# Optimization experiments

Measured on AMD Instinct MI355X. Metric: run time of the kernel, lower is better.

The kernel has to match this reference:

```python
import jax, jax.numpy as jnp
import numpy as np

D = 128        # d_model
B = 32         # graphs in batch
NV = 500       # vars per graph -> 2*NV literals per graph
NL = B * 2 * NV            # 32000 literals
NC_G = 2000                # clauses per graph
NC = B * NC_G              # 64000 clauses
K = 3                      # literals per clause
NE = NC * K                # 192000 edges


def setup_inputs() -> dict:
    key = jax.random.key(0)
    ks = jax.random.split(key, 16)
    s = 1.0 / np.sqrt(D)
    inp = {
        'x_unk': jax.random.uniform(ks[0], (NL, D), dtype=jnp.float32),
        'C_w': jax.random.normal(ks[1], (D,), dtype=jnp.float32) * s,
        'C_b': jax.random.normal(ks[2], (D,), dtype=jnp.float32) * s,
        'Wih_lc': jax.random.normal(ks[3], (4 * D, D), dtype=jnp.float32) * s,
        'Whh_lc': jax.random.normal(ks[4], (4 * D, D), dtype=jnp.float32) * s,
        'bih_lc': jax.random.normal(ks[5], (4 * D,), dtype=jnp.float32) * s,
        'bhh_lc': jax.random.normal(ks[6], (4 * D,), dtype=jnp.float32) * s,
        'Wih_cl': jax.random.normal(ks[7], (4 * D, 2 * D), dtype=jnp.float32) * s,
        'Whh_cl': jax.random.normal(ks[8], (4 * D, D), dtype=jnp.float32) * s,
        'bih_cl': jax.random.normal(ks[9], (4 * D,), dtype=jnp.float32) * s,
        'bhh_cl': jax.random.normal(ks[10], (4 * D,), dtype=jnp.float32) * s,
        'out_w': jax.random.normal(ks[11], (D, 1), dtype=jnp.float32) * s,
        'out_b': jax.random.normal(ks[12], (1,), dtype=jnp.float32) * s,
    }
    rng = np.random.default_rng(0)
    # each clause samples K literals within its own graph
    lit_local = rng.integers(0, 2 * NV, size=(B, NC_G, K))
    offs = (np.arange(B) * 2 * NV)[:, None, None]
    inp['lit_idx'] = jnp.asarray((lit_local + offs).reshape(-1), dtype=jnp.int32)
    inp['clause_idx'] = jnp.asarray(np.repeat(np.arange(NC), K), dtype=jnp.int32)
    inp['l_batch'] = jnp.asarray(np.repeat(np.arange(B), 2 * NV), dtype=jnp.int32)
    # literal flip: swap pos/neg halves within each graph
    loc = np.arange(2 * NV)
    flip_local = np.concatenate([loc[NV:], loc[:NV]])
    inp['flip_perm'] = jnp.asarray(((np.arange(B) * 2 * NV)[:, None] + flip_local[None, :]).reshape(-1), dtype=jnp.int32)
    inp['num_iters'] = 4
    return inp


def _lstm_step(x, h, c, Wih, Whh, bih, bhh):
    # PyTorch LSTM cell: gates ordered [i, f, g, o]
    g = x @ Wih.T + h @ Whh.T + (bih + bhh)
    i, f, gg, o = jnp.split(g, 4, axis=-1)
    c2 = jax.nn.sigmoid(f) * c + jax.nn.sigmoid(i) * jnp.tanh(gg)
    h2 = jax.nn.sigmoid(o) * jnp.tanh(c2)
    return h2, c2


def reference(x_unk, C_w, C_b, Wih_lc, Whh_lc, bih_lc, bhh_lc,
              Wih_cl, Whh_cl, bih_cl, bhh_cl, out_w, out_b,
              clause_idx, lit_idx, l_batch, flip_perm, num_iters):
    n_lits = x_unk.shape[0]
    n_clauses = clause_idx.shape[0] // K
    # init embeddings: x_unk ~ U[0,1); x_c = C_init(1) repeated; cell states zero
    h_l, c_l = x_unk, jnp.zeros_like(x_unk)
    h_c = jnp.broadcast_to(C_w + C_b, (n_clauses, D))  # Linear(1,d) on ones(1)
    c_c = jnp.zeros((n_clauses, D), dtype=x_unk.dtype)
    for _ in range(num_iters):
        # lit -> clause: msg = adj_t @ x_l (SpMM via gather+segment_sum)
        msg_c = jax.ops.segment_sum(h_l[lit_idx], clause_idx, num_segments=n_clauses)
        h_c, c_c = _lstm_step(msg_c, h_c, c_c, Wih_lc, Whh_lc, bih_lc, bhh_lc)
        # clause -> lit: msg = adj_t.T @ x_c, concat with flipped literals
        msg_l = jax.ops.segment_sum(h_c[clause_idx], lit_idx, num_segments=n_lits)
        inp = jnp.concatenate([msg_l, h_l[flip_perm]], axis=-1)  # [NL, 2D]
        h_l, c_l = _lstm_step(inp, h_l, c_l, Wih_cl, Whh_cl, bih_cl, bhh_cl)
    votes = h_l @ out_w + out_b  # [NL, 1]
    sums = jax.ops.segment_sum(votes, l_batch, num_segments=B)
    cnts = jax.ops.segment_sum(jnp.ones((n_lits, 1), votes.dtype), l_batch, num_segments=B)
    vote_reduced = sums / cnts  # global_mean_pool
    return vote_reduced, votes, h_l
```

## Files before the change

### kernel.cpp

```cpp
#include <hip/hip_runtime.h>
#include <hip/hip_bf16.h>

#define D     128
#define NLIT  32000
#define NCLA  64000
#define KLIT  3
#define NEDGE 192000
#define BGR   32
#define ITERS 4
#define LITS_PER_GRAPH 1000

typedef _Float16 f16x8 __attribute__((ext_vector_type(8)));
typedef float    f32x4 __attribute__((ext_vector_type(4)));

__device__ __forceinline__ float sigf(float x)  { return 1.f / (1.f + __expf(-x)); }
__device__ __forceinline__ float tanhft(float x){ return 1.f - 2.f / (__expf(2.f * x) + 1.f); }

__device__ __forceinline__ void async_cp16(const void* g, void* l) {
    __builtin_amdgcn_global_load_lds((const __attribute__((address_space(1))) void*)g,
                                     (__attribute__((address_space(3))) void*)l,
                                     16, 0, 0);
}

__global__ void conv_x_kernel(const float* __restrict__ x, _Float16* __restrict__ o) {
    int t = blockIdx.x * blockDim.x + threadIdx.x;
    if (t >= NLIT * 16) return;
    const float* p = x + t * 8;
    f16x8 v;
#pragma unroll
    for (int i = 0; i < 8; ++i) v[i] = (_Float16)p[i];
    *(f16x8*)((_Float16*)o + t * 8) = v;
}

__global__ void conv_wc_kernel(const float* __restrict__ Wih,
                               const float* __restrict__ Whh,
                               _Float16* __restrict__ Wc) {
    int n = blockIdx.x, k = threadIdx.x;
    float v = (k < 128) ? Wih[n * 128 + k] : Whh[n * 128 + k - 128];
    Wc[n * 256 + k] = (_Float16)v;
}

__global__ void conv_wl_kernel(const float* __restrict__ Wih,
                               const float* __restrict__ Whh,
                               _Float16* __restrict__ Wl) {
    int n = blockIdx.x, k = threadIdx.x;
    float v = (k < 256) ? Wih[n * 256 + k] : Whh[n * 128 + k - 256];
    Wl[n * 384 + k] = (_Float16)v;
}

__global__ void conv_bias_kernel(const float* bih_c, const float* bhh_c, float* bc,
                                 const float* bih_l, const float* bhh_l, float* bl,
                                 const float* C_w, const float* C_b,
                                 _Float16* hc0g) {
    int t = threadIdx.x;
    bc[t] = bih_c[t] + bhh_c[t];
    bl[t] = bih_l[t] + bhh_l[t];
    if (t < 128) hc0g[t] = (_Float16)(C_w[t] + C_b[t]);
}

__global__ void count_edges_kernel(const int* __restrict__ lit_idx,
                                   int* __restrict__ counts) {
    int e = blockIdx.x * blockDim.x + threadIdx.x;
    if (e < NEDGE) atomicAdd(&counts[lit_idx[e]], 1);
}

__global__ __launch_bounds__(256)
void block_sum_kernel(const int* __restrict__ counts, int* __restrict__ bsum) {
    int b = blockIdx.x, t = threadIdx.x;
    int v = counts[b * 256 + t];
    int lane = t & 63, w = t >> 6;
#pragma unroll
    for (int off = 32; off > 0; off >>= 1) v += __shfl_down(v, off, 64);
    __shared__ int ws[4];
    if (lane == 0) ws[w] = v;
    __syncthreads();
    if (t == 0) bsum[b] = ws[0] + ws[1] + ws[2] + ws[3];
}

__global__ void scan_bsum_kernel(const int* __restrict__ bsum,
                                 int* __restrict__ ebsum,
                                 int* __restrict__ starts) {
    __shared__ int s[128];
    int t = threadIdx.x;
    int v = (t < 125) ? bsum[t] : 0;
    s[t] = v;
    __syncthreads();
    for (int off = 1; off < 128; off <<= 1) {
        int y = (t >= off) ? s[t - off] : 0;
        __syncthreads();
        s[t] += y;
        __syncthreads();
    }
    if (t < 125) ebsum[t] = s[t] - v;
    if (t == 0) starts[NLIT] = NEDGE;
}

__global__ __launch_bounds__(256)
void scan_write_kernel(const int* __restrict__ counts,
                       const int* __restrict__ ebsum,
                       int* __restrict__ starts,
                       int* __restrict__ cursor) {
    int b = blockIdx.x, t = threadIdx.x;
    int idx = b * 256 + t;
    int v = counts[idx];
    int lane = t & 63, w = t >> 6;
    int x = v;
#pragma unroll
    for (int off = 1; off < 64; off <<= 1) {
        int y = __shfl_up(x, off, 64);
        if (lane >= off) x += y;
    }
    __shared__ int wsum[4];
    if (lane == 63) wsum[w] = x;
    __syncthreads();
    int woff = 0;
#pragma unroll
    for (int i = 0; i < 4; ++i) if (i < w) woff += wsum[i];
    int g = ebsum[b] + woff + x - v;
    starts[idx] = g;
    cursor[idx] = g;
}

__global__ void fill_csr_kernel(const int* __restrict__ lit_idx,
                                const int* __restrict__ clause_idx,
                                int* __restrict__ cursor,
                                int* __restrict__ edge_clause) {
    int e = blockIdx.x * blockDim.x + threadIdx.x;
    if (e < NEDGE) {
        int l = lit_idx[e];
        int pos = atomicAdd(&cursor[l], 1);
        edge_clause[pos] = clause_idx[e];
    }
}

__global__ void gather_msg_kernel(const _Float16* __restrict__ h_c16,
                                  _Float16* __restrict__ msg16,
                                  const int* __restrict__ starts,
                                  const int* __restrict__ edge_clause) {
    int t = blockIdx.x * blockDim.x + threadIdx.x;
    if (t >= NLIT * 16) return;
    int l = t >> 4;
    int off = (t & 15) * 8;
    int s = starts[l], e = starts[l + 1];
    float a[8];
#pragma unroll
    for (int i = 0; i < 8; ++i) a[i] = 0.f;
    for (int j = s; j < e; ++j) {
        f16x8 v = *(const f16x8*)&h_c16[(size_t)edge_clause[j] * D + off];
#pragma unroll
        for (int i = 0; i < 8; ++i) a[i] += (float)v[i];
    }
    f16x8 o;
#pragma unroll
    for (int i = 0; i < 8; ++i) o[i] = (_Float16)a[i];
    *(f16x8*)&msg16[(size_t)l * D + off] = o;
}

__global__ __launch_bounds__(256, 2)
void clause_mfma_kernel(const _Float16* __restrict__ h_l16,
                        const _Float16* __restrict__ h_c_old,
                        _Float16* __restrict__ h_c_new,
                        float* __restrict__ c_c,
                        const _Float16* __restrict__ Wc,
                        const float* __restrict__ bc,
                        const _Float16* __restrict__ hc0g,
                        const int* __restrict__ lit_idx,
                        int first) {
    __shared__ _Float16 Wl[256 * 32];
    __shared__ _Float16 Al[128 * 32];
    __shared__ int      lidx[384];

    const int tid  = threadIdx.x;
    const int w    = tid >> 6;
    const int lane = tid & 63;
    const int qd   = lane >> 4;
    const int ln   = lane & 15;
    const int bx   = blockIdx.x;
    const int c    = bx & 1;
    const int row0 = (bx >> 1) * 128;

    for (int i = tid; i < 384; i += 256) lidx[i] = lit_idx[row0 * 3 + i];

    f32x4 acc[8][4];
#pragma unroll
    for (int R = 0; R < 8; ++R)
#pragma unroll
        for (int g = 0; g < 4; ++g) { acc[R][g][0]=0.f; acc[R][g][1]=0.f; acc[R][g][2]=0.f; acc[R][g][3]=0.f; }

    for (int ch = 0; ch < 8; ++ch) {
        const int k0 = ch * 32;
        __syncthreads();
        {
            const int nbase = w * 128 + c * 64;
#pragma unroll
            for (int j = 0; j < 4; ++j) {
                int r = 16 * j + (lane >> 2);
                async_cp16(Wc + (nbase + r) * 256 + k0 + (lane & 3) * 8,
                           &Wl[(64 * w + 16 * j) * 32]);
            }
        }
        if (ch < 4) {
#pragma unroll
            for (int s2 = 0; s2 < 2; ++s2) {
                int s   = tid + 256 * s2;
                int m   = s >> 2;
                int off = (s & 3) * 8;
                int kk  = k0 + off;
                f16x8 v0 = *(const f16x8*)&h_l16[(size_t)lidx[3 * m + 0] * D + kk];
                f16x8 v1 = *(const f16x8*)&h_l16[(size_t)lidx[3 * m + 1] * D + kk];
                f16x8 v2 = *(const f16x8*)&h_l16[(size_t)lidx[3 * m + 2] * D + kk];
                f16x8 o;
#pragma unroll
                for (int i = 0; i < 8; ++i) o[i] = (_Float16)((float)v0[i] + (float)v1[i] + (float)v2[i]);
                *(f16x8*)&Al[m * 32 + off] = o;
            }
        } else if (first) {
#pragma unroll
            for (int s2 = 0; s2 < 2; ++s2) {
                int s   = tid + 256 * s2;
                int m   = s >> 2;
                int off = (s & 3) * 8;
                f16x8 v = *(const f16x8*)&hc0g[(k0 - 128) + off];
                *(f16x8*)&Al[m * 32 + off] = v;
            }
        } else {
            int m = 32 * w + (lane >> 2);
            async_cp16(h_c_old + (size_t)(row0 + m) * D + (k0 - 128) + (lane & 3) * 8,
                       &Al[(32 * w) * 32]);
            async_cp16(h_c_old + (size_t)(row0 + m + 16) * D + (k0 - 128) + (lane & 3) * 8,
                       &Al[(32 * w + 16) * 32]);
        }
        __syncthreads();
        f16x8 af[8], bf[4];
#pragma unroll
        for (int R = 0; R < 8; ++R)
            af[R] = *(const f16x8*)&Al[(16 * R + ln) * 32 + qd * 8];
#pragma unroll
        for (int g = 0; g < 4; ++g)
            bf[g] = *(const f16x8*)&Wl[(64 * g + 16 * w + ln) * 32 + qd * 8];
#pragma unroll
        for (int R = 0; R < 8; ++R)
#pragma unroll
            for (int g = 0; g < 4; ++g)
                acc[R][g] = __builtin_amdgcn_mfma_f32_16x16x32_f16(af[R], bf[g], acc[R][g], 0, 0, 0);
    }

    const int dcol = c * 64 + 16 * w + ln;
    const float b0 = bc[dcol], b1 = bc[128 + dcol], b2 = bc[256 + dcol], b3 = bc[384 + dcol];
#pragma unroll
    for (int R = 0; R < 8; ++R) {
#pragma unroll
        for (int r = 0; r < 4; ++r) {
            int m = row0 + 16 * R + qd * 4 + r;
            size_t idx = (size_t)m * D + dcol;
            float gi = acc[R][0][r] + b0;
            float gf = acc[R][1][r] + b1;
            float gg = acc[R][2][r] + b2;
            float go = acc[R][3][r] + b3;
            float cn = sigf(gi) * tanhft(gg);
            if (!first) cn += sigf(gf) * c_c[idx];
            float h  = sigf(go) * tanhft(cn);
            c_c[idx]     = cn;
            h_c_new[idx] = (_Float16)h;
        }
    }
}

__global__ __launch_bounds__(256, 2)
void literal_mfma_kernel(const _Float16* __restrict__ h_old16,
                         const _Float16* __restrict__ msg16,
                         _Float16* __restrict__ h_new16,
                         float* __restrict__ h32,
                         float* __restrict__ c_l,
                         const _Float16* __restrict__ Wl384,
                         const float* __restrict__ bl,
                         const int* __restrict__ flip_perm,
                         int first) {
    __shared__ _Float16 Wl[256 * 32];
    __shared__ _Float16 Al[128 * 32];
    __shared__ int      flip_s[128];

    const int tid  = threadIdx.x;
    const int w    = tid >> 6;
    const int lane = tid & 63;
    const int qd   = lane >> 4;
    const int ln   = lane & 15;
    const int bx   = blockIdx.x;
    const int c    = bx & 1;
    const int row0 = (bx >> 1) * 128;

    if (tid < 128) flip_s[tid] = flip_perm[row0 + tid];

    f32x4 acc[8][4];
#pragma unroll
    for (int R = 0; R < 8; ++R)
#pragma unroll
        for (int g = 0; g < 4; ++g) { acc[R][g][0]=0.f; acc[R][g][1]=0.f; acc[R][g][2]=0.f; acc[R][g][3]=0.f; }

    for (int ch = 0; ch < 12; ++ch) {
        const int k0 = ch * 32;
        __syncthreads();
        {
            const int nbase = w * 128 + c * 64;
#pragma unroll
            for (int j = 0; j < 4; ++j) {
                int r = 16 * j + (lane >> 2);
                async_cp16(Wl384 + (nbase + r) * 384 + k0 + (lane & 3) * 8,
                           &Wl[(64 * w + 16 * j) * 32]);
            }
        }
        {
            int m0  = 32 * w + (lane >> 2);
            int sub = (lane & 3) * 8;
            const _Float16 *g0, *g1;
            if (ch < 4) {
                g0 = msg16 + (size_t)(row0 + m0) * D + k0 + sub;
                g1 = msg16 + (size_t)(row0 + m0 + 16) * D + k0 + sub;
            } else if (ch < 8) {
                g0 = h_old16 + (size_t)flip_s[m0] * D + (k0 - 128) + sub;
                g1 = h_old16 + (size_t)flip_s[m0 + 16] * D + (k0 - 128) + sub;
            } else {
                g0 = h_old16 + (size_t)(row0 + m0) * D + (k0 - 256) + sub;
                g1 = h_old16 + (size_t)(row0 + m0 + 16) * D + (k0 - 256) + sub;
            }
            async_cp16(g0, &Al[(32 * w) * 32]);
            async_cp16(g1, &Al[(32 * w + 16) * 32]);
        }
        __syncthreads();
        f16x8 af[8], bf[4];
#pragma unroll
        for (int R = 0; R < 8; ++R)
            af[R] = *(const f16x8*)&Al[(16 * R + ln) * 32 + qd * 8];
#pragma unroll
        for (int g = 0; g < 4; ++g)
            bf[g] = *(const f16x8*)&Wl[(64 * g + 16 * w + ln) * 32 + qd * 8];
#pragma unroll
        for (int R = 0; R < 8; ++R)
#pragma unroll
            for (int g = 0; g < 4; ++g)
                acc[R][g] = __builtin_amdgcn_mfma_f32_16x16x32_f16(af[R], bf[g], acc[R][g], 0, 0, 0);
    }

    const int dcol = c * 64 + 16 * w + ln;
    const float b0 = bl[dcol], b1 = bl[128 + dcol], b2 = bl[256 + dcol], b3 = bl[384 + dcol];
#pragma unroll
    for (int R = 0; R < 8; ++R) {
#pragma unroll
        for (int r = 0; r < 4; ++r) {
            int m = row0 + 16 * R + qd * 4 + r;
            size_t idx = (size_t)m * D + dcol;
            float gi = acc[R][0][r] + b0;
            float gf = acc[R][1][r] + b1;
            float gg = acc[R][2][r] + b2;
            float go = acc[R][3][r] + b3;
            float cn = sigf(gi) * tanhft(gg);
            if (!first) cn += sigf(gf) * c_l[idx];
            float h  = sigf(go) * tanhft(cn);
            c_l[idx]     = cn;
            h_new16[idx] = (_Float16)h;
            if (h32) h32[idx] = h;
        }
    }
}

__global__ __launch_bounds__(256)
void votes_stage1_kernel(const float* __restrict__ h_l,
                         const float* __restrict__ out_w,
                         const float* __restrict__ out_b,
                         float* __restrict__ votes_out) {
    int w    = threadIdx.x >> 6;
    int lane = threadIdx.x & 63;
    int l    = blockIdx.x * 4 + w;
    if (l >= NLIT) return;
    const float2 v = *(const float2*)&h_l[(size_t)l * D + lane * 2];
    const float2 ww = *(const float2*)&out_w[lane * 2];
    float p = v.x * ww.x + v.y * ww.y;
#pragma unroll
    for (int off = 32; off > 0; off >>= 1) p += __shfl_down(p, off, 64);
    if (lane == 0) votes_out[l] = p + out_b[0];
}

__global__ __launch_bounds__(256)
void votes_stage2_kernel(const float* __restrict__ votes,
                         float* __restrict__ out0) {
    int b = blockIdx.x;
    int t = threadIdx.x;
    const float* base = votes + (size_t)b * LITS_PER_GRAPH;
    float s = 0.f;
    for (int i = t; i < LITS_PER_GRAPH; i += 256) s += base[i];
#pragma unroll
    for (int off = 32; off > 0; off >>= 1) s += __shfl_down(s, off, 64);
    __shared__ float ws[4];
    if ((t & 63) == 0) ws[t >> 6] = s;
    __syncthreads();
    if (t == 0) out0[b] = (ws[0] + ws[1] + ws[2] + ws[3]) / (float)LITS_PER_GRAPH;
}

extern "C" void kernel_launch(void* const* d_in, const int* in_sizes, int n_in,
                              void* d_out, int out_size, void* d_ws, size_t ws_size,
                              hipStream_t stream) {
    (void)in_sizes; (void)n_in; (void)out_size; (void)ws_size;

    const float* x_unk  = (const float*)d_in[0];
    const float* C_w    = (const float*)d_in[1];
    const float* C_b    = (const float*)d_in[2];
    const float* Wih_lc = (const float*)d_in[3];
    const float* Whh_lc = (const float*)d_in[4];
    const float* bih_lc = (const float*)d_in[5];
    const float* bhh_lc = (const float*)d_in[6];
    const float* Wih_cl = (const float*)d_in[7];
    const float* Whh_cl = (const float*)d_in[8];
    const float* bih_cl = (const float*)d_in[9];
    const float* bhh_cl = (const float*)d_in[10];
    const float* out_w  = (const float*)d_in[11];
    const float* out_b  = (const float*)d_in[12];
    const int* lit_idx    = (const int*)d_in[13];
    const int* clause_idx = (const int*)d_in[14];
    const int* flip_perm  = (const int*)d_in[16];

    char* W = (char*)d_ws;
    size_t off = 0;
    auto alloc = [&](size_t bytes) { char* p = W + off; off = (off + bytes + 255) & ~(size_t)255; return p; };
    _Float16* h_l16_0 = (_Float16*)alloc((size_t)NLIT * D * 2);
    _Float16* h_l16_1 = (_Float16*)alloc((size_t)NLIT * D * 2);
    _Float16* h_c16_0 = (_Float16*)alloc((size_t)NCLA * D * 2);
    _Float16* h_c16_1 = (_Float16*)alloc((size_t)NCLA * D * 2);
    _Float16* msg16   = (_Float16*)alloc((size_t)NLIT * D * 2);
    float*    c_l     = (float*)  alloc((size_t)NLIT * D * 4);
    float*    c_c     = (float*)  alloc((size_t)NCLA * D * 4);
    _Float16* Wc16    = (_Float16*)alloc(512 * 256 * 2);
    _Float16* Wl16    = (_Float16*)alloc(512 * 384 * 2);
    float*    bc      = (float*)  alloc(512 * 4);
    float*    bl      = (float*)  alloc(512 * 4);
    _Float16* hc0g    = (_Float16*)alloc(128 * 2);
    int* counts       = (int*)alloc((size_t)NLIT * 4);
    int* starts       = (int*)alloc((size_t)(NLIT + 1) * 4);
    int* cursor       = (int*)alloc((size_t)NLIT * 4);
    int* edge_clause  = (int*)alloc((size_t)NEDGE * 4);
    int* bsum         = (int*)alloc(128 * 4);
    int* ebsum        = (int*)alloc(128 * 4);

    float* out       = (float*)d_out;
    float* out_votes = out + BGR;
    float* out_hl    = out + BGR + NLIT;

    hipMemsetAsync(counts, 0, (size_t)NLIT * 4, stream);

    conv_x_kernel<<<(NLIT * 16 + 255) / 256, 256, 0, stream>>>(x_unk, h_l16_0);
    conv_wc_kernel<<<512, 256, 0, stream>>>(Wih_lc, Whh_lc, Wc16);
    conv_wl_kernel<<<512, 384, 0, stream>>>(Wih_cl, Whh_cl, Wl16);
    conv_bias_kernel<<<1, 512, 0, stream>>>(bih_lc, bhh_lc, bc, bih_cl, bhh_cl, bl,
                                            C_w, C_b, hc0g);

    count_edges_kernel<<<(NEDGE + 255) / 256, 256, 0, stream>>>(lit_idx, counts);
    block_sum_kernel<<<NLIT / 256, 256, 0, stream>>>(counts, bsum);
    scan_bsum_kernel<<<1, 128, 0, stream>>>(bsum, ebsum, starts);
    scan_write_kernel<<<NLIT / 256, 256, 0, stream>>>(counts, ebsum, starts, cursor);
    fill_csr_kernel<<<(NEDGE + 255) / 256, 256, 0, stream>>>(lit_idx, clause_idx,
                                                             cursor, edge_clause);

    const _Float16* hl_old[ITERS] = {h_l16_0, h_l16_1, h_l16_0, h_l16_1};
    _Float16*       hl_new[ITERS] = {h_l16_1, h_l16_0, h_l16_1, h_l16_0};
    const _Float16* hc_old[ITERS] = {h_c16_0, h_c16_1, h_c16_0, h_c16_1};
    _Float16*       hc_new[ITERS] = {h_c16_1, h_c16_0, h_c16_1, h_c16_0};

    for (int it = 0; it < ITERS; ++it) {
        clause_mfma_kernel<<<(NCLA / 128) * 2, 256, 0, stream>>>(
            hl_old[it], hc_old[it], hc_new[it], c_c, Wc16, bc, hc0g, lit_idx,
            it == 0 ? 1 : 0);
        gather_msg_kernel<<<(NLIT * 16 + 255) / 256, 256, 0, stream>>>(
            hc_new[it], msg16, starts, edge_clause);
        literal_mfma_kernel<<<(NLIT / 128) * 2, 256, 0, stream>>>(
            hl_old[it], msg16, hl_new[it],
            (it == ITERS - 1) ? out_hl : (float*)nullptr,
            c_l, Wl16, bl, flip_perm,
            it == 0 ? 1 : 0);
    }

    votes_stage1_kernel<<<NLIT / 4, 256, 0, stream>>>(out_hl, out_w, out_b, out_votes);
    votes_stage2_kernel<<<BGR, 256, 0, stream>>>(out_votes, out);
}
```

Before: 533.4 us.

## Fuse clause-to-literal gather into literal LSTM kernel and register-prefetch weight tiles

Removes the separate gather_msg kernel. The literal MFMA kernel now sums clause embeddings via CSR straight into a full 128x128 swizzled LDS tile before its GEMM loop, so the msg16 round trip through global memory goes away. The clause kernel likewise precomputes the whole 3-literal sum tile up front rather than per chunk. Both kernels replace async global-to-LDS copies with register double-buffered prefetch of the next weight and A chunks, using padded LDS strides. The cost is a larger LDS footprint, which may lower occupancy, and the gather work is now duplicated across the two column-half blocks per row tile.

Result: slower. 654.4 us (+22.7%).

```diff
diff --git a/kernel.cpp b/kernel.cpp
--- a/kernel.cpp
+++ b/kernel.cpp
@@ -15,12 +15,6 @@
 
 __device__ __forceinline__ float sigf(float x)  { return 1.f / (1.f + __expf(-x)); }
 __device__ __forceinline__ float tanhft(float x){ return 1.f - 2.f / (__expf(2.f * x) + 1.f); }
-
-__device__ __forceinline__ void async_cp16(const void* g, void* l) {
-    __builtin_amdgcn_global_load_lds((const __attribute__((address_space(1))) void*)g,
-                                     (__attribute__((address_space(3))) void*)l,
-                                     16, 0, 0);
-}
 
 __global__ void conv_x_kernel(const float* __restrict__ x, _Float16* __restrict__ o) {
     int t = blockIdx.x * blockDim.x + threadIdx.x;
@@ -133,29 +127,6 @@
     }
 }
 
-__global__ void gather_msg_kernel(const _Float16* __restrict__ h_c16,
-                                  _Float16* __restrict__ msg16,
-                                  const int* __restrict__ starts,
-                                  const int* __restrict__ edge_clause) {
-    int t = blockIdx.x * blockDim.x + threadIdx.x;
-    if (t >= NLIT * 16) return;
-    int l = t >> 4;
-    int off = (t & 15) * 8;
-    int s = starts[l], e = starts[l + 1];
-    float a[8];
-#pragma unroll
-    for (int i = 0; i < 8; ++i) a[i] = 0.f;
-    for (int j = s; j < e; ++j) {
-        f16x8 v = *(const f16x8*)&h_c16[(size_t)edge_clause[j] * D + off];
-#pragma unroll
-        for (int i = 0; i < 8; ++i) a[i] += (float)v[i];
-    }
-    f16x8 o;
-#pragma unroll
-    for (int i = 0; i < 8; ++i) o[i] = (_Float16)a[i];
-    *(f16x8*)&msg16[(size_t)l * D + off] = o;
-}
-
 __global__ __launch_bounds__(256, 2)
 void clause_mfma_kernel(const _Float16* __restrict__ h_l16,
                         const _Float16* __restrict__ h_c_old,
@@ -166,8 +137,8 @@
                         const _Float16* __restrict__ hc0g,
                         const int* __restrict__ lit_idx,
                         int first) {
-    __shared__ _Float16 Wl[256 * 32];
-    __shared__ _Float16 Al[128 * 32];
+    __shared__ _Float16 Ag[128 * 128];
+    __shared__ _Float16 Wt[256 * 40];
     __shared__ int      lidx[384];
 
     const int tid  = threadIdx.x;
@@ -175,12 +146,38 @@
     const int lane = tid & 63;
     const int qd   = lane >> 4;
     const int ln   = lane & 15;
-    const int bx   = blockIdx.x;
-    const int c    = bx & 1;
-    const int row0 = (bx >> 1) * 128;
+    const int c    = blockIdx.x & 1;
+    const int row0 = (blockIdx.x >> 1) * 128;
+
+    _Float16* Ac = &Ag[0];
 
     for (int i = tid; i < 384; i += 256) lidx[i] = lit_idx[row0 * 3 + i];
 
+    f16x8 ldW[4];
+#pragma unroll
+    for (int jj = 0; jj < 4; ++jj) {
+        int gg  = tid + 256 * jj;
+        int tr  = gg >> 2, col8 = (gg & 3) * 8;
+        int grow = (tr >> 6) * 128 + c * 64 + (tr & 63);
+        ldW[jj] = *(const f16x8*)&Wc[grow * 256 + col8];
+    }
+    __syncthreads();
+
+#pragma unroll 2
+    for (int i = 0; i < 8; ++i) {
+        int s = tid + 256 * i;
+        int m = s >> 4, j = s & 15;
+        f16x8 v0 = *(const f16x8*)&h_l16[(size_t)lidx[3 * m + 0] * D + j * 8];
+        f16x8 v1 = *(const f16x8*)&h_l16[(size_t)lidx[3 * m + 1] * D + j * 8];
+        f16x8 v2 = *(const f16x8*)&h_l16[(size_t)lidx[3 * m + 2] * D + j * 8];
+        f16x8 o;
+#pragma unroll
+        for (int e = 0; e < 8; ++e)
+            o[e] = (_Float16)((float)v0[e] + (float)v1[e] + (float)v2[e]);
+        *(f16x8*)&Ag[m * 128 + ((j ^ (m & 15)) * 8)] = o;
+    }
+
+    f16x8 ldA[2];
     f32x4 acc[8][4];
 #pragma unroll
     for (int R = 0; R < 8; ++R)
@@ -188,56 +185,55 @@
         for (int g = 0; g < 4; ++g) { acc[R][g][0]=0.f; acc[R][g][1]=0.f; acc[R][g][2]=0.f; acc[R][g][3]=0.f; }
 
     for (int ch = 0; ch < 8; ++ch) {
-        const int k0 = ch * 32;
         __syncthreads();
-        {
-            const int nbase = w * 128 + c * 64;
-#pragma unroll
-            for (int j = 0; j < 4; ++j) {
-                int r = 16 * j + (lane >> 2);
-                async_cp16(Wc + (nbase + r) * 256 + k0 + (lane & 3) * 8,
-                           &Wl[(64 * w + 16 * j) * 32]);
+#pragma unroll
+        for (int jj = 0; jj < 4; ++jj) {
+            int gg = tid + 256 * jj;
+            int tr = gg >> 2, col8 = (gg & 3) * 8;
+            *(f16x8*)&Wt[tr * 40 + col8] = ldW[jj];
+        }
+        if (ch >= 4) {
+#pragma unroll
+            for (int s2 = 0; s2 < 2; ++s2) {
+                int gg = tid + 256 * s2;
+                int r = gg >> 2, col8 = (gg & 3) * 8;
+                *(f16x8*)&Ac[r * 40 + col8] = ldA[s2];
             }
         }
-        if (ch < 4) {
-#pragma unroll
-            for (int s2 = 0; s2 < 2; ++s2) {
-                int s   = tid + 256 * s2;
-                int m   = s >> 2;
-                int off = (s & 3) * 8;
-                int kk  = k0 + off;
-                f16x8 v0 = *(const f16x8*)&h_l16[(size_t)lidx[3 * m + 0] * D + kk];
-                f16x8 v1 = *(const f16x8*)&h_l16[(size_t)lidx[3 * m + 1] * D + kk];
-                f16x8 v2 = *(const f16x8*)&h_l16[(size_t)lidx[3 * m + 2] * D + kk];
-                f16x8 o;
-#pragma unroll
-                for (int i = 0; i < 8; ++i) o[i] = (_Float16)((float)v0[i] + (float)v1[i] + (float)v2[i]);
-                *(f16x8*)&Al[m * 32 + off] = o;
+        if (ch < 7) {
+            const int k0n = (ch + 1) * 32;
+#pragma unroll
+            for (int jj = 0; jj < 4; ++jj) {
+                int gg = tid + 256 * jj;
+                int tr = gg >> 2, col8 = (gg & 3) * 8;
+                int grow = (tr >> 6) * 128 + c * 64 + (tr & 63);
+                ldW[jj] = *(const f16x8*)&Wc[grow * 256 + k0n + col8];
             }
-        } else if (first) {
-#pragma unroll
-            for (int s2 = 0; s2 < 2; ++s2) {
-                int s   = tid + 256 * s2;
-                int m   = s >> 2;
-                int off = (s & 3) * 8;
-                f16x8 v = *(const f16x8*)&hc0g[(k0 - 128) + off];
-                *(f16x8*)&Al[m * 32 + off] = v;
+            if (ch + 1 >= 4) {
+                const int kk = k0n - 128;
+#pragma unroll
+                for (int s2 = 0; s2 < 2; ++s2) {
+                    int gg = tid + 256 * s2;
+                    int r = gg >> 2, col8 = (gg & 3) * 8;
+                    ldA[s2] = first ? *(const f16x8*)&hc0g[kk + col8]
+                                    : *(const f16x8*)&h_c_old[(size_t)(row0 + r) * D + kk + col8];
+                }
             }
-        } else {
-            int m = 32 * w + (lane >> 2);
-            async_cp16(h_c_old + (size_t)(row0 + m) * D + (k0 - 128) + (lane & 3) * 8,
-                       &Al[(32 * w) * 32]);
-            async_cp16(h_c_old + (size_t)(row0 + m + 16) * D + (k0 - 128) + (lane & 3) * 8,
-                       &Al[(32 * w + 16) * 32]);
         }
         __syncthreads();
         f16x8 af[8], bf[4];
-#pragma unroll
-        for (int R = 0; R < 8; ++R)
-            af[R] = *(const f16x8*)&Al[(16 * R + ln) * 32 + qd * 8];
+        if (ch < 4) {
+#pragma unroll
+            for (int R = 0; R < 8; ++R)
+                af[R] = *(const f16x8*)&Ag[(16 * R + ln) * 128 + (((ch * 4 + qd) ^ ln) * 8)];
+        } else {
+#pragma unroll
+            for (int R = 0; R < 8; ++R)
+                af[R] = *(const f16x8*)&Ac[(16 * R + ln) * 40 + qd * 8];
+        }
 #pragma unroll
         for (int g = 0; g < 4; ++g)
-            bf[g] = *(const f16x8*)&Wl[(64 * g + 16 * w + ln) * 32 + qd * 8];
+            bf[g] = *(const f16x8*)&Wt[(64 * g + 16 * w + ln) * 40 + qd * 8];
 #pragma unroll
         for (int R = 0; R < 8; ++R)
 #pragma unroll
@@ -268,16 +264,18 @@
 
 __global__ __launch_bounds__(256, 2)
 void literal_mfma_kernel(const _Float16* __restrict__ h_old16,
-                         const _Float16* __restrict__ msg16,
+                         const _Float16* __restrict__ h_c16,
                          _Float16* __restrict__ h_new16,
                          float* __restrict__ h32,
                          float* __restrict__ c_l,
                          const _Float16* __restrict__ Wl384,
                          const float* __restrict__ bl,
                          const int* __restrict__ flip_perm,
+                         const int* __restrict__ starts,
+                         const int* __restrict__ edge_clause,
                          int first) {
-    __shared__ _Float16 Wl[256 * 32];
-    __shared__ _Float16 Al[128 * 32];
+    __shared__ _Float16 Ag[128 * 128];
+    __shared__ _Float16 Wt[256 * 40];
     __shared__ int      flip_s[128];
 
     const int tid  = threadIdx.x;
@@ -285,12 +283,43 @@
     const int lane = tid & 63;
     const int qd   = lane >> 4;
     const int ln   = lane & 15;
-    const int bx   = blockIdx.x;
-    const int c    = bx & 1;
-    const int row0 = (bx >> 1) * 128;
+    const int c    = blockIdx.x & 1;
+    const int row0 = (blockIdx.x >> 1) * 128;
+
+    _Float16* Ac = &Ag[0];
 
     if (tid < 128) flip_s[tid] = flip_perm[row0 + tid];
 
+    f16x8 ldW[4];
+#pragma unroll
+    for (int jj = 0; jj < 4; ++jj) {
+        int gg  = tid + 256 * jj;
+        int tr  = gg >> 2, col8 = (gg & 3) * 8;
+        int grow = (tr >> 6) * 128 + c * 64 + (tr & 63);
+        ldW[jj] = *(const f16x8*)&Wl384[grow * 384 + col8];
+    }
+
+#pragma unroll 2
+    for (int i = 0; i < 8; ++i) {
+        int s = tid + 256 * i;
+        int m = s >> 4, j = s & 15;
+        int l = row0 + m;
+        int e0 = starts[l], e1 = starts[l + 1];
+        float a[8];
+#pragma unroll
+        for (int e = 0; e < 8; ++e) a[e] = 0.f;
+        for (int p = e0; p < e1; ++p) {
+            f16x8 v = *(const f16x8*)&h_c16[(size_t)edge_clause[p] * D + j * 8];
+#pragma unroll
+            for (int e = 0; e < 8; ++e) a[e] += (float)v[e];
+        }
+        f16x8 o;
+#pragma unroll
+        for (int e = 0; e < 8; ++e) o[e] = (_Float16)a[e];
+        *(f16x8*)&Ag[m * 128 + ((j ^ (m & 15)) * 8)] = o;
+    }
+
+    f16x8 ldA[2];
     f32x4 acc[8][4];
 #pragma unroll
     for (int R = 0; R < 8; ++R)
@@ -298,42 +327,56 @@
         for (int g = 0; g < 4; ++g) { acc[R][g][0]=0.f; acc[R][g][1]=0.f; acc[R][g][2]=0.f; acc[R][g][3]=0.f; }
 
     for (int ch = 0; ch < 12; ++ch) {
-        const int k0 = ch * 32;
         __syncthreads();
-        {
-            const int nbase = w * 128 + c * 64;
-#pragma unroll
-            for (int j = 0; j < 4; ++j) {
-                int r = 16 * j + (lane >> 2);
-                async_cp16(Wl384 + (nbase + r) * 384 + k0 + (lane & 3) * 8,
-                           &Wl[(64 * w + 16 * j) * 32]);
+#pragma unroll
+        for (int jj = 0; jj < 4; ++jj) {
+            int gg = tid + 256 * jj;
+            int tr = gg >> 2, col8 = (gg & 3) * 8;
+            *(f16x8*)&Wt[tr * 40 + col8] = ldW[jj];
+        }
+        if (ch >= 4) {
+#pragma unroll
+            for (int s2 = 0; s2 < 2; ++s2) {
+                int gg = tid + 256 * s2;
+                int r = gg >> 2, col8 = (gg & 3) * 8;
+                *(f16x8*)&Ac[r * 40 + col8] = ldA[s2];
             }
         }
-        {
-            int m0  = 32 * w + (lane >> 2);
-            int sub = (lane & 3) * 8;
-            const _Float16 *g0, *g1;
-            if (ch < 4) {
-                g0 = msg16 + (size_t)(row0 + m0) * D + k0 + sub;
-                g1 = msg16 + (size_t)(row0 + m0 + 16) * D + k0 + sub;
-            } else if (ch < 8) {
-                g0 = h_old16 + (size_t)flip_s[m0] * D + (k0 - 128) + sub;
-                g1 = h_old16 + (size_t)flip_s[m0 + 16] * D + (k0 - 128) + sub;
-            } else {
-                g0 = h_old16 + (size_t)(row0 + m0) * D + (k0 - 256) + sub;
-                g1 = h_old16 + (size_t)(row0 + m0 + 16) * D + (k0 - 256) + sub;
+        if (ch < 11) {
+            const int k0n = (ch + 1) * 32;
+#pragma unroll
+            for (int jj = 0; jj < 4; ++jj) {
+                int gg = tid + 256 * jj;
+                int tr = gg >> 2, col8 = (gg & 3) * 8;
+                int grow = (tr >> 6) * 128 + c * 64 + (tr & 63);
+                ldW[jj] = *(const f16x8*)&Wl384[grow * 384 + k0n + col8];
             }
-            async_cp16(g0, &Al[(32 * w) * 32]);
-            async_cp16(g1, &Al[(32 * w + 16) * 32]);
+            if (ch + 1 >= 4) {
+#pragma unroll
+                for (int s2 = 0; s2 < 2; ++s2) {
+                    int gg = tid + 256 * s2;
+                    int r = gg >> 2, col8 = (gg & 3) * 8;
+                    const _Float16* g;
+                    if (ch + 1 < 8) g = h_old16 + (size_t)flip_s[r] * D + (k0n - 128) + col8;
+                    else            g = h_old16 + (size_t)(row0 + r) * D + (k0n - 256) + col8;
+                    ldA[s2] = *(const f16x8*)g;
+                }
+            }
         }
         __syncthreads();
         f16x8 af[8], bf[4];
-#pragma unroll
-        for (int R = 0; R < 8; ++R)
-            af[R] = *(const f16x8*)&Al[(16 * R + ln) * 32 + qd * 8];
+        if (ch < 4) {
+#pragma unroll
+            for (int R = 0; R < 8; ++R)
+                af[R] = *(const f16x8*)&Ag[(16 * R + ln) * 128 + (((ch * 4 + qd) ^ ln) * 8)];
+        } else {
+#pragma unroll
+            for (int R = 0; R < 8; ++R)
+                af[R] = *(const f16x8*)&Ac[(16 * R + ln) * 40 + qd * 8];
+        }
 #pragma unroll
         for (int g = 0; g < 4; ++g)
-            bf[g] = *(const f16x8*)&Wl[(64 * g + 16 * w + ln) * 32 + qd * 8];
+            bf[g] = *(const f16x8*)&Wt[(64 * g + 16 * w + ln) * 40 + qd * 8];
 #pragma unroll
         for (int R = 0; R < 8; ++R)
 #pragma unroll
@@ -425,7 +468,6 @@
     _Float16* h_l16_1 = (_Float16*)alloc((size_t)NLIT * D * 2);
     _Float16* h_c16_0 = (_Float16*)alloc((size_t)NCLA * D * 2);
     _Float16* h_c16_1 = (_Float16*)alloc((size_t)NCLA * D * 2);
-    _Float16* msg16   = (_Float16*)alloc((size_t)NLIT * D * 2);
     float*    c_l     = (float*)  alloc((size_t)NLIT * D * 4);
     float*    c_c     = (float*)  alloc((size_t)NCLA * D * 4);
     _Float16* Wc16    = (_Float16*)alloc(512 * 256 * 2);
@@ -468,12 +510,10 @@
         clause_mfma_kernel<<<(NCLA / 128) * 2, 256, 0, stream>>>(
             hl_old[it], hc_old[it], hc_new[it], c_c, Wc16, bc, hc0g, lit_idx,
             it == 0 ? 1 : 0);
-        gather_msg_kernel<<<(NLIT * 16 + 255) / 256, 256, 0, stream>>>(
-            hc_new[it], msg16, starts, edge_clause);
         literal_mfma_kernel<<<(NLIT / 128) * 2, 256, 0, stream>>>(
-            hl_old[it], msg16, hl_new[it],
+            hl_old[it], hc_new[it], hl_new[it],
             (it == ITERS - 1) ? out_hl : (float*)nullptr,
-            c_l, Wl16, bl, flip_perm,
+            c_l, Wl16, bl, flip_perm, starts, edge_clause,
             it == 0 ? 1 : 0);
     }
 
```
